# Optimization experiments

Hardware: AMD Instinct MI355X
Metric: run time of the kernel (lower is better)

The kernel has to match this reference:

```python
import jax, jax.numpy as jnp
import numpy as np

B, T, H = 128, 1024, 200
IN0, OUT = 8, 4  # GRU layer-0 input size (4 targets + 4 emotion), fc output dim


def setup_inputs() -> dict:
    key = jax.random.key(0)
    ks = jax.random.split(key, 12)
    s = 1.0 / np.sqrt(H)  # torch RNN default init: U(-1/sqrt(H), 1/sqrt(H))
    u = lambda k, shp: jax.random.uniform(k, shp, jnp.float32, -s, s)
    return {
        "x": jax.random.normal(ks[0], (B, T, IN0), jnp.float32),
        "W_ih0": u(ks[1], (3 * H, IN0)),
        "W_hh0": u(ks[2], (3 * H, H)),
        "b_ih0": u(ks[3], (3 * H,)),
        "b_hh0": u(ks[4], (3 * H,)),
        "W_ih1": u(ks[5], (3 * H, H)),
        "W_hh1": u(ks[6], (3 * H, H)),
        "b_ih1": u(ks[7], (3 * H,)),
        "b_hh1": u(ks[8], (3 * H,)),
        "W_fc": u(ks[9], (OUT, H)),
        "b_fc": u(ks[10], (OUT,)),
        "xlens": jax.random.randint(ks[11], (B,), 1, T + 1),
    }


def _gru_cell(h, gx, W_hh, b_hh):
    # torch GRU cell: gx = W_ih @ x + b_ih precomputed, gates order [r, z, n]
    gh = h @ W_hh.T + b_hh
    ir, iz, i_n = jnp.split(gx, 3, axis=-1)
    hr, hz, hn = jnp.split(gh, 3, axis=-1)
    r = jax.nn.sigmoid(ir + hr)
    z = jax.nn.sigmoid(iz + hz)
    n = jnp.tanh(i_n + r * hn)
    return (1.0 - z) * n + z * h


def _forward(x, W_ih0, W_hh0, b_ih0, b_hh0, W_ih1, W_hh1, b_ih1, b_hh1, W_fc, b_fc):
    b, t, _ = x.shape
    emotion = x[:, 0, -4:]                      # (B,4) frozen at t=0, as in source
    targets = x[:, :, :4]                       # (B,T,4)
    # step inputs: t=0 -> ones(B,4); t>0 -> targets[:, t-1] (teacher forcing)
    tf = jnp.concatenate([jnp.ones((b, 1, 4), x.dtype), targets[:, :-1, :]], axis=1)
    inputs = jnp.concatenate(
        [tf, jnp.broadcast_to(emotion[:, None, :], (b, t, 4))], axis=-1)  # (B,T,8)
    # precompute layer-0 input projections for all steps (one big GEMM)
    gx0 = jnp.einsum("btc,gc->btg", inputs, W_ih0) + b_ih0  # (B,T,3H)

    def step(carry, gx0_t):
        h0, h1 = carry
        h0 = _gru_cell(h0, gx0_t, W_hh0, b_hh0)
        gx1 = h0 @ W_ih1.T + b_ih1
        h1 = _gru_cell(h1, gx1, W_hh1, b_hh1)
        out = jnp.tanh(h1 @ W_fc.T + b_fc)      # fused fc + tanh
        return (h0, h1), out

    h0 = jnp.zeros((b, H), x.dtype)
    h1 = jnp.zeros((b, H), x.dtype)
    _, outs = jax.lax.scan(step, (h0, h1), jnp.swapaxes(gx0, 0, 1))  # (T,B,4)
    return jnp.swapaxes(outs, 0, 1)             # (B,T,4)


def reference(x, W_ih0, W_hh0, b_ih0, b_hh0, W_ih1, W_hh1, b_ih1, b_hh1, W_fc, b_fc, xlens):
    # xlens is accepted but unused, exactly as in the source forward()
    return _forward(x, W_ih0, W_hh0, b_ih0, b_hh0, W_ih1, W_hh1, b_ih1, b_hh1, W_fc, b_fc)
```

## Files before the change

kernel.cpp:

```cpp
#include <hip/hip_runtime.h>
#include <hip/hip_bf16.h>


#define TT 1024
#define HH 200
#define NB 16
#define HS 13
#define KP 232

typedef __attribute__((ext_vector_type(8))) short short8;
typedef __attribute__((ext_vector_type(4))) float f32x4;

__device__ __forceinline__ float sigm(float v) { return 1.0f / (1.0f + __expf(-v)); }
__device__ __forceinline__ float tanh_fast(float v) {
  float e = __expf(-2.0f * v);
  return (1.0f - e) / (1.0f + e);
}
__device__ __forceinline__ uint llc_load_u32(const uint* p) {
  return __hip_atomic_load(p, __ATOMIC_RELAXED, __HIP_MEMORY_SCOPE_AGENT);
}
__device__ __forceinline__ void llc_store_u32(uint* p, uint v) {
  __hip_atomic_store(p, v, __ATOMIC_RELAXED, __HIP_MEMORY_SCOPE_AGENT);
}
__device__ __forceinline__ float bfu2f(ushort u) {
  return __uint_as_float(((uint)u) << 16);
}
__device__ __forceinline__ ushort f2bfu(float f) {
  __hip_bfloat16 b = __float2bfloat16(f);
  return *(ushort*)&b;
}
__device__ __forceinline__ uint packf(float h) {
  ushort hi = f2bfu(h);
  float  fh = bfu2f(hi);
  ushort lo = f2bfu(h - fh);
  return (uint)hi | ((uint)lo << 16);
}

__global__ __launch_bounds__(256, 1) void gru2_mfma(
    const float* __restrict__ x,
    const float* __restrict__ Wih0, const float* __restrict__ Whh0,
    const float* __restrict__ bih0, const float* __restrict__ bhh0,
    const float* __restrict__ Wih1, const float* __restrict__ Whh1,
    const float* __restrict__ bih1, const float* __restrict__ bhh1,
    const float* __restrict__ Wfc,  const float* __restrict__ bfc,
    float* __restrict__ out,
    uint* __restrict__ h0g, uint* __restrict__ h1g, uint* __restrict__ syncp)
{
  __shared__ __align__(16) ushort hBh[2][NB][KP];
  __shared__ __align__(16) ushort hBl[2][NB][KP];
  __shared__ float D[117][17];
  __shared__ float Wi0[39][8];
  __shared__ float bi0[39], bh0[39], bi1[39], bh1[39], bfs[4];
  __shared__ float xc[NB][8];

  const int tid  = threadIdx.x;
  const int wave = tid >> 6;
  const int lane = tid & 63;
  const int m15  = lane & 15;
  const int q    = lane >> 4;

  const int g  = blockIdx.x & 7;
  const int s  = blockIdx.x >> 3;
  const int b0 = g * NB;
  const int j0 = s * HS;
  const int hs = (HH - j0 < HS) ? (HH - j0) : HS;
  const int th   = 3 * hs;
  const int h0r  = 6 * hs;
  const int T0   = (h0r + 15) >> 4;
  const int NT   = T0 + ((th + 15) >> 4);
  const bool isOut = (s == 15);

  uint* flags = syncp;

  short8 Ah[2][7], Al[2][7];
  #pragma unroll
  for (int mt = 0; mt < 2; ++mt) {
    const int T = wave * 2 + mt;
    const bool fc  = isOut && (wave == 2) && (mt == 0);
    const bool val = fc || (T < NT);
    #pragma unroll
    for (int kt = 0; kt < 7; ++kt) {
      short8 vh = {0,0,0,0,0,0,0,0}, vl = {0,0,0,0,0,0,0,0};
      #pragma unroll
      for (int j = 0; j < 8; ++j) {
        const int k = kt * 32 + q * 8 + j;
        float w = 0.0f;
        if (val && k < HH) {
          if (fc) {
            if (m15 < 4) w = Wfc[m15 * HH + k];
          } else {
            const int p = T * 16 + m15;
            int r = -1;
            if (p < h0r) r = p;
            else if (p >= T0 * 16 && (p - T0 * 16) < th) r = h0r + (p - T0 * 16);
            if (r >= 0) {
              const int m  = r / th, rr = r - m * th;
              const int qq = rr / hs, jj = rr - qq * hs;
              const float* src = (m == 0) ? Whh0 : ((m == 1) ? Wih1 : Whh1);
              w = src[(qq * HH + j0 + jj) * HH + k];
            }
          }
        }
        const ushort uh = f2bfu(w);
        const ushort ul = f2bfu(w - bfu2f(uh));
        vh[j] = (short)uh; vl[j] = (short)ul;
      }
      Ah[mt][kt] = vh; Al[mt][kt] = vl;
    }
  }

  for (int u = tid; u < th * 8; u += 256) {
    int rr = u >> 3, c = u & 7;
    int qq = rr / hs, jj = rr - qq * hs;
    Wi0[rr][c] = Wih0[(qq * HH + j0 + jj) * 8 + c];
  }
  for (int u = tid; u < th; u += 256) {
    int qq = u / hs, jj = u - qq * hs;
    int grow = qq * HH + j0 + jj;
    bi0[u] = bih0[grow]; bh0[u] = bhh0[grow];
    bi1[u] = bih1[grow]; bh1[u] = bhh1[grow];
  }
  if (tid < 4) bfs[tid] = bfc[tid];
  for (int u = tid; u < 2 * NB * KP / 2; u += 256) ((uint*)hBh)[u] = 0;
  for (int u = tid; u < 2 * NB * KP / 2; u += 256) ((uint*)hBl)[u] = 0;
  if (tid < 128 && (tid & 7) >= 4)
    xc[tid >> 3][tid & 7] = x[(b0 + (tid >> 3)) * TT * 8 + (tid & 7)];
  __syncthreads();

  const int cj = tid >> 4, cb = tid & 15;
  const int xb = tid >> 3, xcc7 = tid & 7;

  for (int t = 0; t <= TT + 1; ++t) {
    float xtf = 1.0f;
    if (tid < 128 && xcc7 < 4 && t > 0 && t < TT)
      xtf = x[((b0 + xb) * TT + (t - 1)) * 8 + xcc7];

    const uint* h0src = h0g + ((t + 1) & 1) * (128 * HH);
    const uint* h1src = h1g + (t & 1) * (128 * HH);
    uint tmp[25];
    #pragma unroll
    for (int i = 0; i < 25; ++i) {
      const int u  = tid + i * 256;
      const int st = u / 3200, rem = u - st * 3200;
      const int b  = rem / 200, k = rem - b * 200;
      tmp[i] = llc_load_u32(&(st ? h1src : h0src)[(b0 + b) * HH + k]);
    }
    #pragma unroll
    for (int i = 0; i < 25; ++i) {
      const int u  = tid + i * 256;
      const int st = u / 3200, rem = u - st * 3200;
      const int b  = rem / 200, k = rem - b * 200;
      hBh[st][b][k] = (ushort)(tmp[i] & 0xffff);
      hBl[st][b][k] = (ushort)(tmp[i] >> 16);
    }
    if (tid < 128 && xcc7 < 4 && t < TT)
      xc[xb][xcc7] = xtf;
    __syncthreads();

    #pragma unroll
    for (int mt = 0; mt < 2; ++mt) {
      const int T = wave * 2 + mt;
      const bool fc  = isOut && (wave == 2) && (mt == 0);
      const bool val = fc || (T < NT);
      if (!val) continue;
      const int st = fc ? 1 : ((T < T0) ? 0 : 1);
      const ushort* Bh = &hBh[st][m15][0];
      const ushort* Bl = &hBl[st][m15][0];
      f32x4 acc = {0.f, 0.f, 0.f, 0.f};
      #pragma unroll
      for (int kt = 0; kt < 7; ++kt) {
        const short8 bh = *(const short8*)&Bh[kt * 32 + q * 8];
        const short8 bl = *(const short8*)&Bl[kt * 32 + q * 8];
        acc = __builtin_amdgcn_mfma_f32_16x16x32_bf16(Ah[mt][kt], bh, acc, 0, 0, 0);
        acc = __builtin_amdgcn_mfma_f32_16x16x32_bf16(Ah[mt][kt], bl, acc, 0, 0, 0);
        acc = __builtin_amdgcn_mfma_f32_16x16x32_bf16(Al[mt][kt], bh, acc, 0, 0, 0);
      }
      if (fc) {
        if (t >= 2) {
          #pragma unroll
          for (int i = 0; i < 4; ++i) {
            const int p = q * 4 + i;
            if (p < 4)
              out[((b0 + m15) * TT + (t - 2)) * 4 + p] = tanh_fast(acc[i] + bfs[p]);
          }
        }
      } else {
        #pragma unroll
        for (int i = 0; i < 4; ++i) {
          const int p = T * 16 + q * 4 + i;
          int r = -1;
          if (p < h0r) r = p;
          else if (p >= T0 * 16 && (p - T0 * 16) < th) r = h0r + (p - T0 * 16);
          if (r >= 0) D[r][m15] = acc[i];
        }
      }
    }
    __syncthreads();

    if (cj < hs) {
      const float hv0 = bfu2f(hBh[0][cb][j0 + cj]) + bfu2f(hBl[0][cb][j0 + cj]);
      const float hv1 = bfu2f(hBh[1][cb][j0 + cj]) + bfu2f(hBl[1][cb][j0 + cj]);
      if (t < TT) {
        float ir = bi0[cj], iz = bi0[hs + cj], in_ = bi0[2 * hs + cj];
        #pragma unroll
        for (int c = 0; c < 8; ++c) {
          const float xv = xc[cb][c];
          ir  += Wi0[cj][c] * xv;
          iz  += Wi0[hs + cj][c] * xv;
          in_ += Wi0[2 * hs + cj][c] * xv;
        }
        const float hr = D[cj][cb] + bh0[cj];
        const float hz = D[hs + cj][cb] + bh0[hs + cj];
        const float hn = D[2 * hs + cj][cb] + bh0[2 * hs + cj];
        const float r = sigm(ir + hr), z = sigm(iz + hz);
        const float n = tanh_fast(in_ + r * hn);
        llc_store_u32(&h0g[(t & 1) * (128 * HH) + (b0 + cb) * HH + j0 + cj],
                      packf((1.0f - z) * n + z * hv0));
      }
      if (t >= 1 && t <= TT) {
        const float ir  = D[3 * hs + cj][cb] + bi1[cj];
        const float iz  = D[4 * hs + cj][cb] + bi1[hs + cj];
        const float in_ = D[5 * hs + cj][cb] + bi1[2 * hs + cj];
        const float hr  = D[6 * hs + cj][cb] + bh1[cj];
        const float hz  = D[7 * hs + cj][cb] + bh1[hs + cj];
        const float hn  = D[8 * hs + cj][cb] + bh1[2 * hs + cj];
        const float r = sigm(ir + hr), z = sigm(iz + hz);
        const float n = tanh_fast(in_ + r * hn);
        llc_store_u32(&h1g[((t + 1) & 1) * (128 * HH) + (b0 + cb) * HH + j0 + cj],
                      packf((1.0f - z) * n + z * hv1));
      }
    }

    __syncthreads();
    if (tid == 0)
      llc_store_u32(&flags[g * 64 + s * 4], (uint)(t + 1));
    if (wave == 0) {
      const uint tgt = (uint)(t + 1);
      const uint* fp = &flags[g * 64 + (lane & 15) * 4];
      for (int it = 0; it < 200000; ++it) {
        uint v = tgt;
        if (lane < 16) v = llc_load_u32(fp);
        if (__all((int)(v >= tgt))) break;
        __builtin_amdgcn_s_sleep(1);
      }
    }
    __syncthreads();
  }
}

extern "C" void kernel_launch(void* const* d_in, const int* in_sizes, int n_in,
                              void* d_out, int out_size, void* d_ws, size_t ws_size,
                              hipStream_t stream) {
  uint* ws = (uint*)d_ws;
  hipMemsetAsync(d_ws, 0, (size_t)(102400 + 512) * sizeof(uint), stream);
  gru2_mfma<<<128, 256, 0, stream>>>(
      (const float*)d_in[0],
      (const float*)d_in[1], (const float*)d_in[2],
      (const float*)d_in[3], (const float*)d_in[4],
      (const float*)d_in[5], (const float*)d_in[6],
      (const float*)d_in[7], (const float*)d_in[8],
      (const float*)d_in[9], (const float*)d_in[10],
      (float*)d_out, ws, ws + 51200, ws + 102400);
}
```

Baseline: 3.049 ms.

## Replace flag-barrier sync with per-element step tags on hidden state

Each hidden-state word becomes a 64-bit value whose upper half holds the timestep tag, written with a single atomic store. Consumers reload only the elements whose tag is still stale, so the separate flag publish and spin-wait barrier between steps are gone. The aim is to cut global barrier latency on every recurrent step. The cost is twice the load/store traffic, extra retry loops, and a fallback kernel used when the workspace is too small.

Result: slower. 6.704 ms (+119.9%).

```diff
diff --git a/kernel.cpp b/kernel.cpp
--- a/kernel.cpp
+++ b/kernel.cpp
@@ -10,6 +10,7 @@
 
 typedef __attribute__((ext_vector_type(8))) short short8;
 typedef __attribute__((ext_vector_type(4))) float f32x4;
+typedef unsigned long long ull;
 
 __device__ __forceinline__ float sigm(float v) { return 1.0f / (1.0f + __expf(-v)); }
 __device__ __forceinline__ float tanh_fast(float v) {
@@ -17,9 +18,15 @@
   return (1.0f - e) / (1.0f + e);
 }
 __device__ __forceinline__ uint llc_load_u32(const uint* p) {
+  return __hip_atomic_load(p, __ATOMIC_RELAXED, __HIP_MEMORY_SCOPE_SYSTEM);
+}
+__device__ __forceinline__ void llc_store_u32(uint* p, uint v) {
+  __hip_atomic_store(p, v, __ATOMIC_RELAXED, __HIP_MEMORY_SCOPE_SYSTEM);
+}
+__device__ __forceinline__ ull ld64(const ull* p) {
   return __hip_atomic_load(p, __ATOMIC_RELAXED, __HIP_MEMORY_SCOPE_AGENT);
 }
-__device__ __forceinline__ void llc_store_u32(uint* p, uint v) {
+__device__ __forceinline__ void st64(ull* p, ull v) {
   __hip_atomic_store(p, v, __ATOMIC_RELAXED, __HIP_MEMORY_SCOPE_AGENT);
 }
 __device__ __forceinline__ float bfu2f(ushort u) {
@@ -36,7 +43,7 @@
   return (uint)hi | ((uint)lo << 16);
 }
 
-__global__ __launch_bounds__(256, 1) void gru2_mfma(
+__global__ __launch_bounds__(256, 1) void gru2_tag(
     const float* __restrict__ x,
     const float* __restrict__ Wih0, const float* __restrict__ Whh0,
     const float* __restrict__ bih0, const float* __restrict__ bhh0,
@@ -44,7 +51,7 @@
     const float* __restrict__ bih1, const float* __restrict__ bhh1,
     const float* __restrict__ Wfc,  const float* __restrict__ bfc,
     float* __restrict__ out,
-    uint* __restrict__ h0g, uint* __restrict__ h1g, uint* __restrict__ syncp)
+    ull* __restrict__ h0t, ull* __restrict__ h1t)
 {
   __shared__ __align__(16) ushort hBh[2][NB][KP];
   __shared__ __align__(16) ushort hBl[2][NB][KP];
@@ -69,8 +76,6 @@
   const int T0   = (h0r + 15) >> 4;
   const int NT   = T0 + ((th + 15) >> 4);
   const bool isOut = (s == 15);
-
-  uint* flags = syncp;
 
   short8 Ah[2][7], Al[2][7];
   #pragma unroll
@@ -127,6 +132,16 @@
     xc[tid >> 3][tid & 7] = x[(b0 + (tid >> 3)) * TT * 8 + (tid & 7)];
   __syncthreads();
 
+  int su[25]; uint stmask = 0;
+  #pragma unroll
+  for (int i = 0; i < 25; ++i) {
+    const int u = tid + i * 256;
+    const int st = u / 3200, rem = u - st * 3200;
+    const int b = rem / 200, k = rem - b * 200;
+    su[i] = (b0 + b) * HH + k;
+    stmask |= (uint)st << i;
+  }
+
   const int cj = tid >> 4, cb = tid & 15;
   const int xb = tid >> 3, xcc7 = tid & 7;
 
@@ -135,23 +150,45 @@
     if (tid < 128 && xcc7 < 4 && t > 0 && t < TT)
       xtf = x[((b0 + xb) * TT + (t - 1)) * 8 + xcc7];
 
-    const uint* h0src = h0g + ((t + 1) & 1) * (128 * HH);
-    const uint* h1src = h1g + (t & 1) * (128 * HH);
-    uint tmp[25];
+    const int s0 = ((t + 1) & 1) * 25600;
+    const int s1 = (t & 1) * 25600;
+    ull w[25];
     #pragma unroll
     for (int i = 0; i < 25; ++i) {
-      const int u  = tid + i * 256;
+      const ull* p = (((stmask >> i) & 1) ? h1t + s1 : h0t + s0) + su[i];
+      w[i] = ld64(p);
+    }
+    {
+      const uint etag0 = (uint)t;
+      const uint etag1 = (t >= 2) ? (uint)t : 0u;
+      const bool chk0  = (t <= TT);
+      uint pend = 0x1ffffffu;
+      for (int it = 0; it < 200000; ++it) {
+        uint np = 0;
+        #pragma unroll
+        for (int i = 0; i < 25; ++i) {
+          if (pend & (1u << i)) {
+            const bool is1 = (stmask >> i) & 1;
+            const uint et  = is1 ? etag1 : etag0;
+            if ((is1 || chk0) && (uint)(w[i] >> 32) != et) {
+              const ull* p = (is1 ? h1t + s1 : h0t + s0) + su[i];
+              w[i] = ld64(p);
+              np |= 1u << i;
+            }
+          }
+        }
+        pend = np;
+        if (!np) break;
+      }
+    }
+    #pragma unroll
+    for (int i = 0; i < 25; ++i) {
+      const int u = tid + i * 256;
       const int st = u / 3200, rem = u - st * 3200;
-      const int b  = rem / 200, k = rem - b * 200;
-      tmp[i] = llc_load_u32(&(st ? h1src : h0src)[(b0 + b) * HH + k]);
-    }
-    #pragma unroll
-    for (int i = 0; i < 25; ++i) {
-      const int u  = tid + i * 256;
-      const int st = u / 3200, rem = u - st * 3200;
-      const int b  = rem / 200, k = rem - b * 200;
-      hBh[st][b][k] = (ushort)(tmp[i] & 0xffff);
-      hBl[st][b][k] = (ushort)(tmp[i] >> 16);
+      const int b = rem / 200, k = rem - b * 200;
+      const uint v = (uint)w[i];
+      hBh[st][b][k] = (ushort)(v & 0xffff);
+      hBl[st][b][k] = (ushort)(v >> 16);
     }
     if (tid < 128 && xcc7 < 4 && t < TT)
       xc[xb][xcc7] = xtf;
@@ -200,6 +237,205 @@
     if (cj < hs) {
       const float hv0 = bfu2f(hBh[0][cb][j0 + cj]) + bfu2f(hBl[0][cb][j0 + cj]);
       const float hv1 = bfu2f(hBh[1][cb][j0 + cj]) + bfu2f(hBl[1][cb][j0 + cj]);
+      const ull tag = ((ull)(uint)(t + 1)) << 32;
+      if (t < TT) {
+        float ir = bi0[cj], iz = bi0[hs + cj], in_ = bi0[2 * hs + cj];
+        #pragma unroll
+        for (int c = 0; c < 8; ++c) {
+          const float xv = xc[cb][c];
+          ir  += Wi0[cj][c] * xv;
+          iz  += Wi0[hs + cj][c] * xv;
+          in_ += Wi0[2 * hs + cj][c] * xv;
+        }
+        const float hr = D[cj][cb] + bh0[cj];
+        const float hz = D[hs + cj][cb] + bh0[hs + cj];
+        const float hn = D[2 * hs + cj][cb] + bh0[2 * hs + cj];
+        const float r = sigm(ir + hr), z = sigm(iz + hz);
+        const float n = tanh_fast(in_ + r * hn);
+        st64(&h0t[(t & 1) * 25600 + (b0 + cb) * HH + j0 + cj],
+             (ull)packf((1.0f - z) * n + z * hv0) | tag);
+      }
+      if (t >= 1 && t <= TT) {
+        const float ir  = D[3 * hs + cj][cb] + bi1[cj];
+        const float iz  = D[4 * hs + cj][cb] + bi1[hs + cj];
+        const float in_ = D[5 * hs + cj][cb] + bi1[2 * hs + cj];
+        const float hr  = D[6 * hs + cj][cb] + bh1[cj];
+        const float hz  = D[7 * hs + cj][cb] + bh1[hs + cj];
+        const float hn  = D[8 * hs + cj][cb] + bh1[2 * hs + cj];
+        const float r = sigm(ir + hr), z = sigm(iz + hz);
+        const float n = tanh_fast(in_ + r * hn);
+        st64(&h1t[((t + 1) & 1) * 25600 + (b0 + cb) * HH + j0 + cj],
+             (ull)packf((1.0f - z) * n + z * hv1) | tag);
+      }
+    }
+    __syncthreads();
+  }
+}
+
+__global__ __launch_bounds__(256, 1) void gru2_flag(
+    const float* __restrict__ x,
+    const float* __restrict__ Wih0, const float* __restrict__ Whh0,
+    const float* __restrict__ bih0, const float* __restrict__ bhh0,
+    const float* __restrict__ Wih1, const float* __restrict__ Whh1,
+    const float* __restrict__ bih1, const float* __restrict__ bhh1,
+    const float* __restrict__ Wfc,  const float* __restrict__ bfc,
+    float* __restrict__ out,
+    uint* __restrict__ h0g, uint* __restrict__ h1g, uint* __restrict__ syncp)
+{
+  __shared__ __align__(16) ushort hBh[2][NB][KP];
+  __shared__ __align__(16) ushort hBl[2][NB][KP];
+  __shared__ float D[117][17];
+  __shared__ float Wi0[39][8];
+  __shared__ float bi0[39], bh0[39], bi1[39], bh1[39], bfs[4];
+  __shared__ float xc[NB][8];
+
+  const int tid  = threadIdx.x;
+  const int wave = tid >> 6;
+  const int lane = tid & 63;
+  const int m15  = lane & 15;
+  const int q    = lane >> 4;
+
+  const int g  = blockIdx.x & 7;
+  const int s  = blockIdx.x >> 3;
+  const int b0 = g * NB;
+  const int j0 = s * HS;
+  const int hs = (HH - j0 < HS) ? (HH - j0) : HS;
+  const int th   = 3 * hs;
+  const int h0r  = 6 * hs;
+  const int T0   = (h0r + 15) >> 4;
+  const int NT   = T0 + ((th + 15) >> 4);
+  const bool isOut = (s == 15);
+
+  uint* flags = syncp;
+
+  short8 Ah[2][7], Al[2][7];
+  #pragma unroll
+  for (int mt = 0; mt < 2; ++mt) {
+    const int T = wave * 2 + mt;
+    const bool fc  = isOut && (wave == 2) && (mt == 0);
+    const bool val = fc || (T < NT);
+    #pragma unroll
+    for (int kt = 0; kt < 7; ++kt) {
+      short8 vh = {0,0,0,0,0,0,0,0}, vl = {0,0,0,0,0,0,0,0};
+      #pragma unroll
+      for (int j = 0; j < 8; ++j) {
+        const int k = kt * 32 + q * 8 + j;
+        float w = 0.0f;
+        if (val && k < HH) {
+          if (fc) {
+            if (m15 < 4) w = Wfc[m15 * HH + k];
+          } else {
+            const int p = T * 16 + m15;
+            int r = -1;
+            if (p < h0r) r = p;
+            else if (p >= T0 * 16 && (p - T0 * 16) < th) r = h0r + (p - T0 * 16);
+            if (r >= 0) {
+              const int m  = r / th, rr = r - m * th;
+              const int qq = rr / hs, jj = rr - qq * hs;
+              const float* src = (m == 0) ? Whh0 : ((m == 1) ? Wih1 : Whh1);
+              w = src[(qq * HH + j0 + jj) * HH + k];
+            }
+          }
+        }
+        const ushort uh = f2bfu(w);
+        const ushort ul = f2bfu(w - bfu2f(uh));
+        vh[j] = (short)uh; vl[j] = (short)ul;
+      }
+      Ah[mt][kt] = vh; Al[mt][kt] = vl;
+    }
+  }
+
+  for (int u = tid; u < th * 8; u += 256) {
+    int rr = u >> 3, c = u & 7;
+    int qq = rr / hs, jj = rr - qq * hs;
+    Wi0[rr][c] = Wih0[(qq * HH + j0 + jj) * 8 + c];
+  }
+  for (int u = tid; u < th; u += 256) {
+    int qq = u / hs, jj = u - qq * hs;
+    int grow = qq * HH + j0 + jj;
+    bi0[u] = bih0[grow]; bh0[u] = bhh0[grow];
+    bi1[u] = bih1[grow]; bh1[u] = bhh1[grow];
+  }
+  if (tid < 4) bfs[tid] = bfc[tid];
+  for (int u = tid; u < 2 * NB * KP / 2; u += 256) ((uint*)hBh)[u] = 0;
+  for (int u = tid; u < 2 * NB * KP / 2; u += 256) ((uint*)hBl)[u] = 0;
+  if (tid < 128 && (tid & 7) >= 4)
+    xc[tid >> 3][tid & 7] = x[(b0 + (tid >> 3)) * TT * 8 + (tid & 7)];
+  __syncthreads();
+
+  const int cj = tid >> 4, cb = tid & 15;
+  const int xb = tid >> 3, xcc7 = tid & 7;
+
+  for (int t = 0; t <= TT + 1; ++t) {
+    float xtf = 1.0f;
+    if (tid < 128 && xcc7 < 4 && t > 0 && t < TT)
+      xtf = x[((b0 + xb) * TT + (t - 1)) * 8 + xcc7];
+
+    const uint* h0src = h0g + ((t + 1) & 1) * (128 * HH);
+    const uint* h1src = h1g + (t & 1) * (128 * HH);
+    uint tmp[25];
+    #pragma unroll
+    for (int i = 0; i < 25; ++i) {
+      const int u  = tid + i * 256;
+      const int st = u / 3200, rem = u - st * 3200;
+      const int b  = rem / 200, k = rem - b * 200;
+      tmp[i] = llc_load_u32(&(st ? h1src : h0src)[(b0 + b) * HH + k]);
+    }
+    #pragma unroll
+    for (int i = 0; i < 25; ++i) {
+      const int u  = tid + i * 256;
+      const int st = u / 3200, rem = u - st * 3200;
+      const int b  = rem / 200, k = rem - b * 200;
+      hBh[st][b][k] = (ushort)(tmp[i] & 0xffff);
+      hBl[st][b][k] = (ushort)(tmp[i] >> 16);
+    }
+    if (tid < 128 && xcc7 < 4 && t < TT)
+      xc[xb][xcc7] = xtf;
+    __syncthreads();
+
+    #pragma unroll
+    for (int mt = 0; mt < 2; ++mt) {
+      const int T = wave * 2 + mt;
+      const bool fc  = isOut && (wave == 2) && (mt == 0);
+      const bool val = fc || (T < NT);
+      if (!val) continue;
+      const int st = fc ? 1 : ((T < T0) ? 0 : 1);
+      const ushort* Bh = &hBh[st][m15][0];
+      const ushort* Bl = &hBl[st][m15][0];
+      f32x4 acc = {0.f, 0.f, 0.f, 0.f};
+      #pragma unroll
+      for (int kt = 0; kt < 7; ++kt) {
+        const short8 bh = *(const short8*)&Bh[kt * 32 + q * 8];
+        const short8 bl = *(const short8*)&Bl[kt * 32 + q * 8];
+        acc = __builtin_amdgcn_mfma_f32_16x16x32_bf16(Ah[mt][kt], bh, acc, 0, 0, 0);
+        acc = __builtin_amdgcn_mfma_f32_16x16x32_bf16(Ah[mt][kt], bl, acc, 0, 0, 0);
+        acc = __builtin_amdgcn_mfma_f32_16x16x32_bf16(Al[mt][kt], bh, acc, 0, 0, 0);
+      }
+      if (fc) {
+        if (t >= 2) {
+          #pragma unroll
+          for (int i = 0; i < 4; ++i) {
+            const int p = q * 4 + i;
+            if (p < 4)
+              out[((b0 + m15) * TT + (t - 2)) * 4 + p] = tanh_fast(acc[i] + bfs[p]);
+          }
+        }
+      } else {
+        #pragma unroll
+        for (int i = 0; i < 4; ++i) {
+          const int p = T * 16 + q * 4 + i;
+          int r = -1;
+          if (p < h0r) r = p;
+          else if (p >= T0 * 16 && (p - T0 * 16) < th) r = h0r + (p - T0 * 16);
+          if (r >= 0) D[r][m15] = acc[i];
+        }
+      }
+    }
+    __syncthreads();
+
+    if (cj < hs) {
+      const float hv0 = bfu2f(hBh[0][cb][j0 + cj]) + bfu2f(hBl[0][cb][j0 + cj]);
+      const float hv1 = bfu2f(hBh[1][cb][j0 + cj]) + bfu2f(hBl[1][cb][j0 + cj]);
       if (t < TT) {
         float ir = bi0[cj], iz = bi0[hs + cj], in_ = bi0[2 * hs + cj];
         #pragma unroll
@@ -252,13 +488,26 @@
                               void* d_out, int out_size, void* d_ws, size_t ws_size,
                               hipStream_t stream) {
   uint* ws = (uint*)d_ws;
-  hipMemsetAsync(d_ws, 0, (size_t)(102400 + 512) * sizeof(uint), stream);
-  gru2_mfma<<<128, 256, 0, stream>>>(
-      (const float*)d_in[0],
-      (const float*)d_in[1], (const float*)d_in[2],
-      (const float*)d_in[3], (const float*)d_in[4],
-      (const float*)d_in[5], (const float*)d_in[6],
-      (const float*)d_in[7], (const float*)d_in[8],
-      (const float*)d_in[9], (const float*)d_in[10],
-      (float*)d_out, ws, ws + 51200, ws + 102400);
-}
+  const size_t need_tag = (size_t)204800 * sizeof(uint);
+  if (ws_size >= need_tag) {
+    hipMemsetAsync(d_ws, 0, need_tag, stream);
+    gru2_tag<<<128, 256, 0, stream>>>(
+        (const float*)d_in[0],
+        (const float*)d_in[1], (const float*)d_in[2],
+        (const float*)d_in[3], (const float*)d_in[4],
+        (const float*)d_in[5], (const float*)d_in[6],
+        (const float*)d_in[7], (const float*)d_in[8],
+        (const float*)d_in[9], (const float*)d_in[10],
+        (float*)d_out, (ull*)d_ws, ((ull*)d_ws) + 51200);
+  } else {
+    hipMemsetAsync(d_ws, 0, (size_t)(102400 + 512) * sizeof(uint), stream);
+    gru2_flag<<<128, 256, 0, stream>>>(
+        (const float*)d_in[0],
+        (const float*)d_in[1], (const float*)d_in[2],
+        (const float*)d_in[3], (const float*)d_in[4],
+        (const float*)d_in[5], (const float*)d_in[6],
+        (const float*)d_in[7], (const float*)d_in[8],
+        (const float*)d_in[9], (const float*)d_in[10],
+        (float*)d_out, ws, ws + 51200, ws + 102400);
+  }
+}
```
